# Performance work log

Measured on AMD Instinct MI355X. Metric: run time of the kernel, lower is better.

## Reference

```python
import jax, jax.numpy as jnp
import numpy as np

N_HEAD = 12
N_EMBD = 768

def setup_inputs() -> dict:
    key = jax.random.key(0)
    ks = jax.random.split(key, 5)
    B, T, C = 4, 2048, N_EMBD
    x = jax.random.normal(ks[0], (B, T, C), dtype=jnp.float32)
    # PyTorch Linear default init ~ U(-1/sqrt(fan_in), 1/sqrt(fan_in)); use small normals for a clean baseline
    s = 1.0 / np.sqrt(C)
    W_attn = jax.random.uniform(ks[1], (C, 3 * C), minval=-s, maxval=s, dtype=jnp.float32)
    b_attn = jax.random.uniform(ks[2], (3 * C,), minval=-s, maxval=s, dtype=jnp.float32)
    W_o = jax.random.uniform(ks[3], (C, C), minval=-s, maxval=s, dtype=jnp.float32)
    b_o = jax.random.uniform(ks[4], (C,), minval=-s, maxval=s, dtype=jnp.float32)
    return {"x": x, "W_attn": W_attn, "b_attn": b_attn, "W_o": W_o, "b_o": b_o}

def reference(x, W_attn, b_attn, W_o, b_o):
    B, T, C = x.shape
    H = N_HEAD
    D = C // H  # head dim
    qkv = x @ W_attn + b_attn                      # [B,T,3C]
    q, k, v = jnp.split(qkv, 3, axis=-1)           # each [B,T,C]
    q = q.reshape(B, T, H, D).transpose(0, 2, 1, 3)  # [B,H,T,D]
    k = k.reshape(B, T, H, D).transpose(0, 2, 1, 3)
    v = v.reshape(B, T, H, D).transpose(0, 2, 1, 3)
    att = jnp.einsum('bhqd,bhkd->bhqk', q, k) / jnp.sqrt(jnp.asarray(D, x.dtype))
    causal = jnp.tril(jnp.ones((T, T), dtype=bool))
    att = jnp.where(causal, att, jnp.asarray(-jnp.inf, att.dtype))
    att = jax.nn.softmax(att, axis=-1)             # dropout=0.0 -> identity
    y = jnp.einsum('bhqk,bhkd->bhqd', att, v)      # [B,H,T,D]
    y = y.transpose(0, 2, 1, 3).reshape(B, T, C)   # [B,T,C]
    return y @ W_o + b_o
```

## Files before the change

kernel.cpp:

```cpp
#include <hip/hip_runtime.h>
#include <hip/hip_bf16.h>

#define NHEAD 12
#define TSEQ 2048
#define CEMB 768
#define DHEAD 64
#define NBATCH 4

typedef __attribute__((ext_vector_type(8))) short bf16x8;
typedef __attribute__((ext_vector_type(4))) float f32x4;

__device__ __forceinline__ ushort f2bf(float f) {
  union { float f; unsigned u; } v; v.f = f;
  unsigned u = v.u;
  u += 0x7FFFu + ((u >> 16) & 1u);
  return (ushort)(u >> 16);
}

__device__ __forceinline__ unsigned cvt_pk_bf16(float lo, float hi) {
  unsigned r;
  asm("v_cvt_pk_bf16_f32 %0, %1, %2" : "=v"(r) : "v"(lo), "v"(hi));
  return r;
}

__device__ __forceinline__ float exp2_raw(float x) {
  float r;
  asm("v_exp_f32 %0, %1" : "=v"(r) : "v"(x));
  return r;
}

__global__ __launch_bounds__(256)
void prep(const float* __restrict__ x, ushort* __restrict__ xb,
          const float* __restrict__ Wa, ushort* __restrict__ WaT,
          const float* __restrict__ Wo, ushort* __restrict__ WoT)
{
  __shared__ float tile[32][33];
  const int bid = blockIdx.x, t = threadIdx.x;
  if (bid < 3072) {
    int i = (bid * 256 + t) * 8;
    float4 v0 = *(const float4*)(x + i);
    float4 v1 = *(const float4*)(x + i + 4);
    bf16x8 wv;
    wv[0] = (short)f2bf(v0.x); wv[1] = (short)f2bf(v0.y);
    wv[2] = (short)f2bf(v0.z); wv[3] = (short)f2bf(v0.w);
    wv[4] = (short)f2bf(v1.x); wv[5] = (short)f2bf(v1.y);
    wv[6] = (short)f2bf(v1.z); wv[7] = (short)f2bf(v1.w);
    *(bf16x8*)(xb + i) = wv;
    return;
  }
  const int b2 = bid - 3072;
  const int bx = b2 % 96, by = b2 / 96;
  const int tx = t & 31, ty = t >> 5;
  const float* src; ushort* dst; int C, c0;
  if (bx < 72) { src = Wa; dst = WaT; C = 3 * CEMB; c0 = bx * 32; }
  else         { src = Wo; dst = WoT; C = CEMB;     c0 = (bx - 72) * 32; }
  const int r0 = by * 32;
#pragma unroll
  for (int j = 0; j < 4; ++j)
    tile[ty + j * 8][tx] = src[(size_t)(r0 + ty + j * 8) * C + c0 + tx];
  __syncthreads();
#pragma unroll
  for (int j = 0; j < 4; ++j)
    dst[(size_t)(c0 + ty + j * 8) * CEMB + r0 + tx] = f2bf(tile[tx][ty + j * 8]);
}

template<int EPI>
__global__ __launch_bounds__(256)
void gemm_bf16(const ushort* __restrict__ A, const ushort* __restrict__ BT,
               const float* __restrict__ bias, float* __restrict__ outF,
               ushort* __restrict__ qd, ushort* __restrict__ kd, ushort* __restrict__ vd,
               int M, int N, int K)
{
  __shared__ __align__(16) char smem[32768];
  const int t = threadIdx.x;
  const int lane = t & 63, wv = t >> 6;
  const int cc = lane & 15, gg = lane >> 4;
  const int m0 = blockIdx.y * 128, n0 = blockIdx.x * 128;
  const int wm = (wv >> 1) * 64, wn = (wv & 1) * 64;

  const int o0 = wv * 1024 + lane * 16;
  const int o1 = o0 + 4096;
  const int r0s = o0 >> 6, s0s = (o0 >> 4) & 3;
  const int r1s = o1 >> 6, s1s = (o1 >> 4) & 3;
  const size_t Kb = (size_t)K * 2;
  const char* a0p = (const char*)A  + (size_t)(m0 + r0s) * Kb + ((s0s ^ ((r0s >> 1) & 3)) << 4);
  const char* a1p = (const char*)A  + (size_t)(m0 + r1s) * Kb + ((s1s ^ ((r1s >> 1) & 3)) << 4);
  const char* b0p = (const char*)BT + (size_t)(n0 + r0s) * Kb + ((s0s ^ ((r0s >> 1) & 3)) << 4);
  const char* b1p = (const char*)BT + (size_t)(n0 + r1s) * Kb + ((s1s ^ ((r1s >> 1) & 3)) << 4);

  auto stage_g = [&](int p, int kb) {
    char* As = smem + p * 16384;
    char* Bs = As + 8192;
    __builtin_amdgcn_global_load_lds(
        (const __attribute__((address_space(1))) unsigned*)(a0p + kb),
        (__attribute__((address_space(3))) unsigned*)(As + wv * 1024), 16, 0, 0);
    __builtin_amdgcn_global_load_lds(
        (const __attribute__((address_space(1))) unsigned*)(a1p + kb),
        (__attribute__((address_space(3))) unsigned*)(As + wv * 1024 + 4096), 16, 0, 0);
    __builtin_amdgcn_global_load_lds(
        (const __attribute__((address_space(1))) unsigned*)(b0p + kb),
        (__attribute__((address_space(3))) unsigned*)(Bs + wv * 1024), 16, 0, 0);
    __builtin_amdgcn_global_load_lds(
        (const __attribute__((address_space(1))) unsigned*)(b1p + kb),
        (__attribute__((address_space(3))) unsigned*)(Bs + wv * 1024 + 4096), 16, 0, 0);
  };

  f32x4 acc[4][4];
#pragma unroll
  for (int i = 0; i < 4; ++i)
#pragma unroll
    for (int j = 0; j < 4; ++j) acc[i][j] = (f32x4){0.f, 0.f, 0.f, 0.f};

  const int KB = K * 2;
  stage_g(0, 0);
  asm volatile("s_waitcnt vmcnt(0)" ::: "memory");
  __syncthreads();
  int p = 0;
  for (int kb = 0; kb < KB; kb += 64) {
    if (kb + 64 < KB) stage_g(p ^ 1, kb + 64);
    const char* As = smem + p * 16384;
    const char* Bs = As + 8192;
    bf16x8 fa[4], fb[4];
#pragma unroll
    for (int i = 0; i < 4; ++i) {
      const int r = wm + i * 16 + cc;
      fa[i] = *(const bf16x8*)(As + r * 64 + ((gg ^ ((r >> 1) & 3)) << 4));
    }
#pragma unroll
    for (int j = 0; j < 4; ++j) {
      const int r = wn + j * 16 + cc;
      fb[j] = *(const bf16x8*)(Bs + r * 64 + ((gg ^ ((r >> 1) & 3)) << 4));
    }
    __builtin_amdgcn_s_setprio(1);
#pragma unroll
    for (int i = 0; i < 4; ++i)
#pragma unroll
      for (int j = 0; j < 4; ++j)
        acc[i][j] = __builtin_amdgcn_mfma_f32_16x16x32_bf16(fa[i], fb[j], acc[i][j], 0, 0, 0);
    __builtin_amdgcn_s_setprio(0);
    asm volatile("s_waitcnt vmcnt(0)" ::: "memory");
    __syncthreads();
    p ^= 1;
  }

#pragma unroll
  for (int i = 0; i < 4; ++i) {
#pragma unroll
    for (int j = 0; j < 4; ++j) {
      int gm0 = m0 + wm + i * 16 + gg * 4;
      int gn  = n0 + wn + j * 16 + cc;
      float bv = bias[gn];
      if (EPI == 0) {
#pragma unroll
        for (int e = 0; e < 4; ++e)
          outF[(size_t)(gm0 + e) * N + gn] = acc[i][j][e] + bv;
      } else {
        int which = gn / CEMB;
        int r = gn - which * CEMB;
        int hh = r >> 6, dd = r & 63;
        int tt0 = gm0 & (TSEQ - 1), bb = gm0 >> 11;
        if (which == 2) {
          ushort* dstv = vd + ((size_t)((bb * NHEAD + hh) * DHEAD + dd)) * TSEQ + tt0;
          uint2 pw;
          pw.x = cvt_pk_bf16(acc[i][j][0] + bv, acc[i][j][1] + bv);
          pw.y = cvt_pk_bf16(acc[i][j][2] + bv, acc[i][j][3] + bv);
          *(uint2*)dstv = pw;
        } else {
          ushort* dst = which == 0 ? qd : kd;
          float sc = (which == 0) ? 0.125f * 1.4426950408889634f : 1.0f;
#pragma unroll
          for (int e = 0; e < 4; ++e)
            dst[(size_t)((bb * NHEAD + hh) * TSEQ + tt0 + e) * DHEAD + dd] =
                f2bf((acc[i][j][e] + bv) * sc);
        }
      }
    }
  }
}

__global__ __launch_bounds__(256)
void attn_fwd(const ushort* __restrict__ qg, const ushort* __restrict__ kg,
              const ushort* __restrict__ vTg, ushort* __restrict__ ybb)
{
  __shared__ __align__(16) char smem[49152];
  const int t = threadIdx.x, lane = t & 63, w = t >> 6;
  const int cc = lane & 15, gg = lane >> 4;
  const int NT = TSEQ / 64;
  const int L = blockIdx.x;
  const int r9 = L >> 3;
  const int bx = r9 & 15;
  const int bh = (L & 7) + 8 * (r9 >> 4);
  const int b = bh / NHEAD, h = bh - b * NHEAD;

  const char* Kg = (const char*)(kg + (size_t)bh * TSEQ * DHEAD);
  const char* Vg = (const char*)(vTg + (size_t)bh * TSEQ * DHEAD);

  const int srow = lane >> 3;
  const int ssw  = ((lane & 7) * 16) ^ (srow << 4);

  ushort* Pw = (ushort*)(smem + 32768 + w * 4096);
  const int sw8 = (cc & 7) << 3;

  bf16x8 ones;
#pragma unroll
  for (int i = 0; i < 8; ++i) ones[i] = (short)0x3F80;

  auto stageK = [&](int pb, int kt) {
#pragma unroll
    for (int i = 0; i < 2; ++i) {
      const int c = w * 2 + i;
      const char* gk = Kg + (size_t)(kt * 64 + c * 8 + srow) * 128 + ssw;
      __builtin_amdgcn_global_load_lds(
          (const __attribute__((address_space(1))) unsigned*)gk,
          (__attribute__((address_space(3))) unsigned*)(smem + pb * 8192 + c * 1024),
          16, 0, 0);
    }
  };
  auto stageV = [&](int pb, int kt) {
#pragma unroll
    for (int i = 0; i < 2; ++i) {
      const int c = w * 2 + i;
      const char* gv = Vg + (size_t)(c * 8 + srow) * (TSEQ * 2) + (size_t)kt * 128 + ssw;
      __builtin_amdgcn_global_load_lds(
          (const __attribute__((address_space(1))) unsigned*)gv,
          (__attribute__((address_space(3))) unsigned*)(smem + 16384 + pb * 8192 + c * 1024),
          16, 0, 0);
    }
  };

  int p = 0;
  for (int pass = 0; pass < 2; ++pass) {
    const int qt = pass ? (NT - 1 - bx) : bx;
    const int qrow0 = qt * 64 + w * 16;

    const ushort* Qp = qg + ((size_t)bh * TSEQ + qrow0) * DHEAD;
    bf16x8 fq0 = *(const bf16x8*)(Qp + cc * DHEAD + 8 * gg);
    bf16x8 fq1 = *(const bf16x8*)(Qp + cc * DHEAD + 32 + 8 * gg);

    f32x4 o[4];
    f32x4 l4 = (f32x4){0.f, 0.f, 0.f, 0.f};
#pragma unroll
    for (int i = 0; i < 4; ++i) o[i] = (f32x4){0.f, 0.f, 0.f, 0.f};
    float m = 0.f;

    stageK(p, 0);
    asm volatile("s_waitcnt vmcnt(0)" ::: "memory");
    __syncthreads();

    for (int kt = 0; kt <= qt; ++kt) {
      if (kt < qt) stageK(p ^ 1, kt + 1);
      stageV(p, kt);

      const char* Kl = smem + p * 8192;
      f32x4 st[4];
#pragma unroll
      for (int ct = 0; ct < 4; ++ct) st[ct] = (f32x4){0.f, 0.f, 0.f, 0.f};
      __builtin_amdgcn_s_setprio(1);
#pragma unroll
      for (int ct = 0; ct < 4; ++ct) {
        const int r = ct * 16 + cc;
        const char* kb = Kl + r * 128;
        bf16x8 fk0 = *(const bf16x8*)(kb + ((gg * 16) ^ ((r & 7) << 4)));
        bf16x8 fk1 = *(const bf16x8*)(kb + ((64 + gg * 16) ^ ((r & 7) << 4)));
        st[ct] = __builtin_amdgcn_mfma_f32_16x16x32_bf16(fk0, fq0, st[ct], 0, 0, 0);
        st[ct] = __builtin_amdgcn_mfma_f32_16x16x32_bf16(fk1, fq1, st[ct], 0, 0, 0);
      }

      if (kt > 0) {
        const char* Vprev = smem + 16384 + (p ^ 1) * 8192;
        const ushort* Pprev = Pw + (p ^ 1) * 1024;
#pragma unroll
        for (int kc = 0; kc < 2; ++kc) {
          bf16x8 pb = *(const bf16x8*)&Pprev[cc * 64 + ((kc * 32 + 8 * gg) ^ sw8)];
          l4 = __builtin_amdgcn_mfma_f32_16x16x32_bf16(ones, pb, l4, 0, 0, 0);
#pragma unroll
          for (int dt = 0; dt < 4; ++dt) {
            const int rd = dt * 16 + cc;
            bf16x8 fv = *(const bf16x8*)(Vprev + rd * 128 + ((kc * 64 + gg * 16) ^ ((rd & 7) << 4)));
            o[dt] = __builtin_amdgcn_mfma_f32_16x16x32_bf16(fv, pb, o[dt], 0, 0, 0);
          }
        }
      }
      __builtin_amdgcn_s_setprio(0);

      if (kt == qt) {
#pragma unroll
        for (int ct = 0; ct < 4; ++ct)
#pragma unroll
          for (int e = 0; e < 4; ++e)
            if (ct * 16 + gg * 4 + e > w * 16 + cc) st[ct][e] = -1e30f;
      }
      f32x4 pe[4];
#pragma unroll
      for (int ct = 0; ct < 4; ++ct)
#pragma unroll
        for (int e = 0; e < 4; ++e) pe[ct][e] = exp2_raw(st[ct][e] - m);
#pragma unroll
      for (int ct = 0; ct < 4; ++ct) {
        uint2 pw;
        pw.x = cvt_pk_bf16(pe[ct][0], pe[ct][1]);
        pw.y = cvt_pk_bf16(pe[ct][2], pe[ct][3]);
        *(uint2*)&Pw[p * 1024 + cc * 64 + ((ct * 16 + gg * 4) ^ sw8)] = pw;
      }
      float ml = fmaxf(fmaxf(st[0][0], st[0][1]), st[0][2]);
      ml = fmaxf(fmaxf(ml, st[0][3]), fmaxf(st[1][0], st[1][1]));
      ml = fmaxf(fmaxf(ml, st[1][2]), fmaxf(st[1][3], st[2][0]));
      ml = fmaxf(fmaxf(ml, st[2][1]), fmaxf(st[2][2], st[2][3]));
      ml = fmaxf(fmaxf(ml, st[3][0]), fmaxf(st[3][1], st[3][2]));
      ml = fmaxf(ml, st[3][3]);
      ml = fmaxf(ml, __shfl_xor(ml, 16, 64));
      ml = fmaxf(ml, __shfl_xor(ml, 32, 64));
      if (!__all(ml - m <= 11.54f)) {
        float mn = fmaxf(m, ml);
        float al = exp2_raw(m - mn);
#pragma unroll
        for (int dt = 0; dt < 4; ++dt)
#pragma unroll
          for (int e = 0; e < 4; ++e) o[dt][e] *= al;
#pragma unroll
        for (int e = 0; e < 4; ++e) l4[e] *= al;
#pragma unroll
        for (int ct = 0; ct < 4; ++ct) {
#pragma unroll
          for (int e = 0; e < 4; ++e) pe[ct][e] *= al;
          uint2 pw;
          pw.x = cvt_pk_bf16(pe[ct][0], pe[ct][1]);
          pw.y = cvt_pk_bf16(pe[ct][2], pe[ct][3]);
          *(uint2*)&Pw[p * 1024 + cc * 64 + ((ct * 16 + gg * 4) ^ sw8)] = pw;
        }
        m = mn;
      }

      asm volatile("s_waitcnt vmcnt(0)" ::: "memory");
      __syncthreads();
      p ^= 1;
    }

    {
      const char* Vlast = smem + 16384 + (p ^ 1) * 8192;
      const ushort* Plast = Pw + (p ^ 1) * 1024;
#pragma unroll
      for (int kc = 0; kc < 2; ++kc) {
        bf16x8 pb = *(const bf16x8*)&Plast[cc * 64 + ((kc * 32 + 8 * gg) ^ sw8)];
        l4 = __builtin_amdgcn_mfma_f32_16x16x32_bf16(ones, pb, l4, 0, 0, 0);
#pragma unroll
        for (int dt = 0; dt < 4; ++dt) {
          const int rd = dt * 16 + cc;
          bf16x8 fv = *(const bf16x8*)(Vlast + rd * 128 + ((kc * 64 + gg * 16) ^ ((rd & 7) << 4)));
          o[dt] = __builtin_amdgcn_mfma_f32_16x16x32_bf16(fv, pb, o[dt], 0, 0, 0);
        }
      }
    }

    float inv = 1.0f / l4[0];
    ushort* yrow = ybb + (size_t)(b * TSEQ + qrow0 + cc) * CEMB + h * DHEAD;
#pragma unroll
    for (int dt = 0; dt < 4; ++dt) {
      uint2 pw;
      pw.x = cvt_pk_bf16(o[dt][0] * inv, o[dt][1] * inv);
      pw.y = cvt_pk_bf16(o[dt][2] * inv, o[dt][3] * inv);
      *(uint2*)(yrow + dt * 16 + gg * 4) = pw;
    }
  }
}

extern "C" void kernel_launch(void* const* d_in, const int* in_sizes, int n_in,
                              void* d_out, int out_size, void* d_ws, size_t ws_size,
                              hipStream_t stream)
{
  (void)in_sizes; (void)n_in; (void)out_size; (void)ws_size;
  const float* x  = (const float*)d_in[0];
  const float* Wa = (const float*)d_in[1];
  const float* ba = (const float*)d_in[2];
  const float* Wo = (const float*)d_in[3];
  const float* bo = (const float*)d_in[4];
  float* out = (float*)d_out;

  char* p = (char*)d_ws;
  ushort* WaT  = (ushort*)p; p += (size_t)3 * CEMB * CEMB * 2;
  ushort* WoT  = (ushort*)p; p += (size_t)CEMB * CEMB * 2;
  ushort* xb   = (ushort*)p; p += (size_t)NBATCH * TSEQ * CEMB * 2;
  ushort* qb   = (ushort*)p; p += (size_t)NBATCH * NHEAD * TSEQ * DHEAD * 2;
  ushort* kb   = (ushort*)p; p += (size_t)NBATCH * NHEAD * TSEQ * DHEAD * 2;
  ushort* vT   = (ushort*)p; p += (size_t)NBATCH * NHEAD * TSEQ * DHEAD * 2;
  ushort* yb   = (ushort*)p; p += (size_t)NBATCH * TSEQ * CEMB * 2;

  prep<<<3072 + 96 * 24, 256, 0, stream>>>(x, xb, Wa, WaT, Wo, WoT);
  gemm_bf16<1><<<dim3(3 * CEMB / 128, NBATCH * TSEQ / 128), 256, 0, stream>>>(
      xb, WaT, ba, nullptr, qb, kb, vT, NBATCH * TSEQ, 3 * CEMB, CEMB);
  attn_fwd<<<dim3(TSEQ / 128 * NBATCH * NHEAD), 256, 0, stream>>>(qb, kb, vT, yb);
  gemm_bf16<0><<<dim3(CEMB / 128, NBATCH * TSEQ / 128), 256, 0, stream>>>(
      yb, WoT, bo, out, nullptr, nullptr, nullptr, NBATCH * TSEQ, CEMB, CEMB);
}
```

Before: 132.4 us.

## Keep softmax P in registers via permlane32 swap instead of LDS round-trip

The attention kernel no longer writes the bf16 probability tile P to shared memory and reads it back for the PV MFMA. It converts P in registers, rearranges it across lane halves with v_permlane32_swap, and reorders the V fragment reads so the K-dimension permutation matches. This removes LDS stores and loads of P and cuts shared memory from 48KB to 32KB, which may allow more blocks per CU. In exchange, V reads become two 8-byte loads instead of one 16-byte load, and P stays live in extra registers across the loop.

```diff
diff --git a/kernel.cpp b/kernel.cpp
--- a/kernel.cpp
+++ b/kernel.cpp
@@ -9,6 +9,7 @@
 
 typedef __attribute__((ext_vector_type(8))) short bf16x8;
 typedef __attribute__((ext_vector_type(4))) float f32x4;
+typedef __attribute__((ext_vector_type(4))) unsigned u32x4;
 
 __device__ __forceinline__ ushort f2bf(float f) {
   union { float f; unsigned u; } v; v.f = f;
@@ -27,6 +28,10 @@
   float r;
   asm("v_exp_f32 %0, %1" : "=v"(r) : "v"(x));
   return r;
+}
+
+__device__ __forceinline__ void permswap(unsigned& a, unsigned& b) {
+  asm("v_permlane32_swap_b32 %0, %1" : "+v"(a), "+v"(b));
 }
 
 __global__ __launch_bounds__(256)
@@ -182,7 +187,7 @@
 void attn_fwd(const ushort* __restrict__ qg, const ushort* __restrict__ kg,
               const ushort* __restrict__ vTg, ushort* __restrict__ ybb)
 {
-  __shared__ __align__(16) char smem[49152];
+  __shared__ __align__(16) char smem[32768];
   const int t = threadIdx.x, lane = t & 63, w = t >> 6;
   const int cc = lane & 15, gg = lane >> 4;
   const int NT = TSEQ / 64;
@@ -198,9 +203,6 @@
   const int srow = lane >> 3;
   const int ssw  = ((lane & 7) * 16) ^ (srow << 4);
 
-  ushort* Pw = (ushort*)(smem + 32768 + w * 4096);
-  const int sw8 = (cc & 7) << 3;
-
   bf16x8 ones;
 #pragma unroll
   for (int i = 0; i < 8; ++i) ones[i] = (short)0x3F80;
@@ -228,6 +230,17 @@
     }
   };
 
+  auto readV = [&](const char* Vbuf, int rd, int kc) -> bf16x8 {
+    const int c1 = kc * 64 + (gg >> 1) * 32;
+    const int o8 = (gg & 1) * 8;
+    const int sx = (rd & 7) << 4;
+    const char* vrow = Vbuf + rd * 128;
+    uint2 v0 = *(const uint2*)(vrow + (c1 ^ sx) + o8);
+    uint2 v1 = *(const uint2*)(vrow + ((c1 + 16) ^ sx) + o8);
+    u32x4 fv = {v0.x, v0.y, v1.x, v1.y};
+    return __builtin_bit_cast(bf16x8, fv);
+  };
+
   int p = 0;
   for (int pass = 0; pass < 2; ++pass) {
     const int qt = pass ? (NT - 1 - bx) : bx;
@@ -242,6 +255,8 @@
 #pragma unroll
     for (int i = 0; i < 4; ++i) o[i] = (f32x4){0.f, 0.f, 0.f, 0.f};
     float m = 0.f;
+    u32x4 pbf[2];
+    pbf[0] = (u32x4){0, 0, 0, 0}; pbf[1] = (u32x4){0, 0, 0, 0};
 
     stageK(p, 0);
     asm volatile("s_waitcnt vmcnt(0)" ::: "memory");
@@ -268,15 +283,13 @@
 
       if (kt > 0) {
         const char* Vprev = smem + 16384 + (p ^ 1) * 8192;
-        const ushort* Pprev = Pw + (p ^ 1) * 1024;
 #pragma unroll
         for (int kc = 0; kc < 2; ++kc) {
-          bf16x8 pb = *(const bf16x8*)&Pprev[cc * 64 + ((kc * 32 + 8 * gg) ^ sw8)];
+          bf16x8 pb = __builtin_bit_cast(bf16x8, pbf[kc]);
           l4 = __builtin_amdgcn_mfma_f32_16x16x32_bf16(ones, pb, l4, 0, 0, 0);
 #pragma unroll
           for (int dt = 0; dt < 4; ++dt) {
-            const int rd = dt * 16 + cc;
-            bf16x8 fv = *(const bf16x8*)(Vprev + rd * 128 + ((kc * 64 + gg * 16) ^ ((rd & 7) << 4)));
+            bf16x8 fv = readV(Vprev, dt * 16 + cc, kc);
             o[dt] = __builtin_amdgcn_mfma_f32_16x16x32_bf16(fv, pb, o[dt], 0, 0, 0);
           }
         }
@@ -295,13 +308,6 @@
       for (int ct = 0; ct < 4; ++ct)
 #pragma unroll
         for (int e = 0; e < 4; ++e) pe[ct][e] = exp2_raw(st[ct][e] - m);
-#pragma unroll
-      for (int ct = 0; ct < 4; ++ct) {
-        uint2 pw;
-        pw.x = cvt_pk_bf16(pe[ct][0], pe[ct][1]);
-        pw.y = cvt_pk_bf16(pe[ct][2], pe[ct][3]);
-        *(uint2*)&Pw[p * 1024 + cc * 64 + ((ct * 16 + gg * 4) ^ sw8)] = pw;
-      }
       float ml = fmaxf(fmaxf(st[0][0], st[0][1]), st[0][2]);
       ml = fmaxf(fmaxf(ml, st[0][3]), fmaxf(st[1][0], st[1][1]));
       ml = fmaxf(fmaxf(ml, st[1][2]), fmaxf(st[1][3], st[2][0]));
@@ -320,15 +326,20 @@
 #pragma unroll
         for (int e = 0; e < 4; ++e) l4[e] *= al;
 #pragma unroll
-        for (int ct = 0; ct < 4; ++ct) {
+        for (int ct = 0; ct < 4; ++ct)
 #pragma unroll
           for (int e = 0; e < 4; ++e) pe[ct][e] *= al;
-          uint2 pw;
-          pw.x = cvt_pk_bf16(pe[ct][0], pe[ct][1]);
-          pw.y = cvt_pk_bf16(pe[ct][2], pe[ct][3]);
-          *(uint2*)&Pw[p * 1024 + cc * 64 + ((ct * 16 + gg * 4) ^ sw8)] = pw;
-        }
         m = mn;
+      }
+      {
+        unsigned wx0 = cvt_pk_bf16(pe[0][0], pe[0][1]), wy0 = cvt_pk_bf16(pe[0][2], pe[0][3]);
+        unsigned wx1 = cvt_pk_bf16(pe[1][0], pe[1][1]), wy1 = cvt_pk_bf16(pe[1][2], pe[1][3]);
+        unsigned wx2 = cvt_pk_bf16(pe[2][0], pe[2][1]), wy2 = cvt_pk_bf16(pe[2][2], pe[2][3]);
+        unsigned wx3 = cvt_pk_bf16(pe[3][0], pe[3][1]), wy3 = cvt_pk_bf16(pe[3][2], pe[3][3]);
+        permswap(wx0, wx1); permswap(wy0, wy1);
+        permswap(wx2, wx3); permswap(wy2, wy3);
+        pbf[0] = (u32x4){wx0, wy0, wx1, wy1};
+        pbf[1] = (u32x4){wx2, wy2, wx3, wy3};
       }
 
       asm volatile("s_waitcnt vmcnt(0)" ::: "memory");
@@ -338,15 +349,13 @@
 
     {
       const char* Vlast = smem + 16384 + (p ^ 1) * 8192;
-      const ushort* Plast = Pw + (p ^ 1) * 1024;
 #pragma unroll
       for (int kc = 0; kc < 2; ++kc) {
-        bf16x8 pb = *(const bf16x8*)&Plast[cc * 64 + ((kc * 32 + 8 * gg) ^ sw8)];
+        bf16x8 pb = __builtin_bit_cast(bf16x8, pbf[kc]);
         l4 = __builtin_amdgcn_mfma_f32_16x16x32_bf16(ones, pb, l4, 0, 0, 0);
 #pragma unroll
         for (int dt = 0; dt < 4; ++dt) {
-          const int rd = dt * 16 + cc;
-          bf16x8 fv = *(const bf16x8*)(Vlast + rd * 128 + ((kc * 64 + gg * 16) ^ ((rd & 7) << 4)));
+          bf16x8 fv = readV(Vlast, dt * 16 + cc, kc);
           o[dt] = __builtin_amdgcn_mfma_f32_16x16x32_bf16(fv, pb, o[dt], 0, 0, 0);
         }
       }
```

Result: no change. 133.7 us (+1.0%).
